# Performance work log

Hardware: AMD Instinct MI355X
Metric: run time of the kernel (lower is better)

## Reference

```python
import jax, jax.numpy as jnp
import numpy as np

HIDDEN = 1280
NUM_HEADS = 20
HEAD_DIM = HIDDEN // NUM_HEADS
B, S = 2, 2048


def setup_inputs() -> dict:
    key = jax.random.key(0)
    k1, k2, k3, k4, k5 = jax.random.split(key, 5)
    scale_in = 1.0 / np.sqrt(HIDDEN)
    return {
        "x": jax.random.normal(k1, (B, S, HIDDEN), dtype=jnp.float32),
        "w_attn": jax.random.normal(k2, (HIDDEN, 3 * HIDDEN), dtype=jnp.float32) * scale_in,
        "b_attn": jax.random.normal(k3, (3 * HIDDEN,), dtype=jnp.float32) * 0.02,
        "w_proj": jax.random.normal(k4, (HIDDEN, HIDDEN), dtype=jnp.float32) * scale_in,
        "b_proj": jax.random.normal(k5, (HIDDEN,), dtype=jnp.float32) * 0.02,
    }


def reference(x, w_attn, b_attn, w_proj, b_proj):
    b, s, _ = x.shape
    scale = 1.0 / np.sqrt(HEAD_DIM)
    qkv = x @ w_attn + b_attn                      # [B,S,3H]
    q, k, v = jnp.split(qkv, 3, axis=-1)

    def heads(t):  # [B,S,H] -> [B,nh,S,hd]
        return t.reshape(b, s, NUM_HEADS, HEAD_DIM).transpose(0, 2, 1, 3)

    q, k, v = heads(q), heads(k), heads(v)
    attn = jnp.einsum("bhqd,bhkd->bhqk", q, k) * scale
    causal = jnp.tril(jnp.ones((s, s), dtype=bool))
    attn = jnp.where(causal, attn, jnp.float32(-jnp.inf))
    attn = jax.nn.softmax(attn, axis=-1)           # dropout = identity (eval)
    out = jnp.einsum("bhqk,bhkd->bhqd", attn, v)
    out = out.transpose(0, 2, 1, 3).reshape(b, s, HIDDEN)
    return out @ w_proj + b_proj
```

## Files before the change

kernel.cpp:

```cpp
#include <hip/hip_runtime.h>

typedef unsigned short u16;
typedef __attribute__((ext_vector_type(8))) short bf16x8;
typedef __attribute__((ext_vector_type(4))) float f32x4;
typedef __attribute__((ext_vector_type(4))) unsigned short u16x4;

#define MFMA16 __builtin_amdgcn_mfma_f32_16x16x32_bf16

__device__ __forceinline__ u16 f2bf(float f) {
  unsigned int u = __float_as_uint(f);
  u += 0x7fff + ((u >> 16) & 1);
  return (u16)(u >> 16);
}

__device__ __forceinline__ float vexp2(float x) {
  float r; asm("v_exp_f32 %0, %1" : "=v"(r) : "v"(x)); return r;
}

template<int CTRL>
__device__ __forceinline__ float dppf(float v) {
  return __int_as_float(__builtin_amdgcn_update_dpp(0, __float_as_int(v), CTRL, 0xF, 0xF, true));
}
__device__ __forceinline__ float rowmax16(float v) {
  v = fmaxf(v, dppf<0xB1>(v));
  v = fmaxf(v, dppf<0x4E>(v));
  v = fmaxf(v, dppf<0x141>(v));
  v = fmaxf(v, dppf<0x140>(v));
  return v;
}
__device__ __forceinline__ float rowsum16(float v) {
  v += dppf<0xB1>(v);
  v += dppf<0x4E>(v);
  v += dppf<0x141>(v);
  v += dppf<0x140>(v);
  return v;
}

__device__ __forceinline__ void gload_lds16(const void* g, void* l) {
  __builtin_amdgcn_global_load_lds((__attribute__((address_space(1))) void*)g,
                                   (__attribute__((address_space(3))) void*)l,
                                   16, 0, 0);
}

__global__ void k_cast(const float* __restrict__ src, u16* __restrict__ dst, int n4) {
  int i = blockIdx.x * 256 + threadIdx.x;
  if (i >= n4) return;
  const float4 v = reinterpret_cast<const float4*>(src)[i];
  u16x4 o = {f2bf(v.x), f2bf(v.y), f2bf(v.z), f2bf(v.w)};
  reinterpret_cast<u16x4*>(dst)[i] = o;
}

__global__ void k_transpose_cast(const float* __restrict__ src, u16* __restrict__ dst,
                                 int R, int C) {
  __shared__ float tile[64][65];
  const int t = threadIdx.x;
  const int c0 = blockIdx.x * 64, r0 = blockIdx.y * 64;
#pragma unroll
  for (int i = 0; i < 16; ++i) {
    int e = i * 256 + t;
    int r = e >> 6, c = e & 63;
    tile[r][c] = src[(size_t)(r0 + r) * C + (c0 + c)];
  }
  __syncthreads();
#pragma unroll
  for (int i = 0; i < 16; ++i) {
    int e = i * 256 + t;
    int r = e >> 6, c = e & 63;
    dst[(size_t)(c0 + r) * R + (r0 + c)] = f2bf(tile[c][r]);
  }
}

__global__ __launch_bounds__(256, 2) void k_gemm_qkv(
    const u16* __restrict__ A, const u16* __restrict__ Bt,
    const float* __restrict__ bias,
    u16* __restrict__ qo, u16* __restrict__ ko, u16* __restrict__ vt) {
  constexpr int K = 1280;
  __shared__ u16 Alds[128 * 64];
  __shared__ u16 Blds[128 * 64];
  const int t = threadIdx.x;
  const int lane = t & 63, wave = t >> 6;
  const int wr = wave >> 1, wc = wave & 1;
  const int l15 = lane & 15, lhi = lane >> 4;
  const int m0 = blockIdx.x * 128, n0 = blockIdx.y * 128;

  f32x4 acc[4][4];
#pragma unroll
  for (int mi = 0; mi < 4; ++mi)
#pragma unroll
    for (int ni = 0; ni < 4; ++ni) acc[mi][ni] = f32x4{0.f, 0.f, 0.f, 0.f};

  const int srow = t >> 3;
  const int scol = (t & 7) * 8;
  const u16* Ag = A + (size_t)(m0 + srow) * K + scol;
  const u16* Bg = Bt + (size_t)(n0 + srow) * K + scol;
  char* Al = (char*)Alds + wave * 1024;
  char* Bl = (char*)Blds + wave * 1024;

  for (int k0 = 0; k0 < K; k0 += 64) {
    __syncthreads();
#pragma unroll
    for (int it = 0; it < 4; ++it) {
      gload_lds16(Ag + (it * 32) * K + k0, Al + it * 4096);
      gload_lds16(Bg + (it * 32) * K + k0, Bl + it * 4096);
    }
    asm volatile("s_waitcnt vmcnt(0)" ::: "memory");
    __syncthreads();
    const u16* Ab = Alds + (wr * 64 + l15) * 64 + lhi * 8;
    const u16* Bb = Blds + (wc * 64 + l15) * 64 + lhi * 8;
    bf16x8 af[4][2], bfv[4][2];
#pragma unroll
    for (int x = 0; x < 4; ++x) {
      af[x][0] = *(const bf16x8*)(Ab + x * 1024);
      af[x][1] = *(const bf16x8*)(Ab + x * 1024 + 32);
      bfv[x][0] = *(const bf16x8*)(Bb + x * 1024);
      bfv[x][1] = *(const bf16x8*)(Bb + x * 1024 + 32);
    }
#pragma unroll
    for (int mi = 0; mi < 4; ++mi)
#pragma unroll
      for (int ni = 0; ni < 4; ++ni) {
        acc[mi][ni] = MFMA16(af[mi][0], bfv[ni][0], acc[mi][ni], 0, 0, 0);
        acc[mi][ni] = MFMA16(af[mi][1], bfv[ni][1], acc[mi][ni], 0, 0, 0);
      }
  }

  const int which = n0 >= 2560 ? 2 : (n0 >= 1280 ? 1 : 0);
  const int bbq = m0 >> 11;
  const int sbase = (m0 & 2047) + wr * 64;
  if (which < 2) {
    u16* outp = which == 0 ? qo : ko;
#pragma unroll
    for (int ni = 0; ni < 4; ++ni) {
      const int n_abs = n0 + wc * 64 + ni * 16 + l15;
      const int nn = n_abs - which * 1280;
      const int h = nn >> 6, d = nn & 63;
      const float bv = bias[n_abs];
#pragma unroll
      for (int mi = 0; mi < 4; ++mi) {
#pragma unroll
        for (int i = 0; i < 4; ++i) {
          const int ss = sbase + mi * 16 + lhi * 4 + i;
          outp[(((size_t)(bbq * 20 + h) * 2048 + ss) << 6) + d] = f2bf(acc[mi][ni][i] + bv);
        }
      }
    }
  } else {
#pragma unroll
    for (int ni = 0; ni < 4; ++ni) {
      const int n_abs = n0 + wc * 64 + ni * 16 + l15;
      const int nn = n_abs - 2560;
      const int h = nn >> 6, d = nn & 63;
      const float bv = bias[n_abs];
      u16* vrow = vt + ((size_t)(bbq * 20 + h) * 64 + d) * 2048;
#pragma unroll
      for (int mi = 0; mi < 4; ++mi) {
        const int ss = sbase + mi * 16 + lhi * 4;
        u16x4 pk = {f2bf(acc[mi][ni][0] + bv), f2bf(acc[mi][ni][1] + bv),
                    f2bf(acc[mi][ni][2] + bv), f2bf(acc[mi][ni][3] + bv)};
        *(u16x4*)(vrow + ss) = pk;
      }
    }
  }
}

__global__ __launch_bounds__(256, 2) void k_gemm_proj(
    const u16* __restrict__ A, const u16* __restrict__ Bt,
    const float* __restrict__ bias, float* __restrict__ out) {
  constexpr int K = 1280;
  __shared__ u16 Alds[128 * 64];
  __shared__ u16 Blds[128 * 64];
  const int t = threadIdx.x;
  const int lane = t & 63, wave = t >> 6;
  const int wr = wave >> 1, wc = wave & 1;
  const int l15 = lane & 15, lhi = lane >> 4;
  const int m0 = blockIdx.x * 128, n0 = blockIdx.y * 128;

  f32x4 acc[4][4];
#pragma unroll
  for (int mi = 0; mi < 4; ++mi)
#pragma unroll
    for (int ni = 0; ni < 4; ++ni) acc[mi][ni] = f32x4{0.f, 0.f, 0.f, 0.f};

  const int srow = t >> 3;
  const int scol = (t & 7) * 8;
  const u16* Ag = A + (size_t)(m0 + srow) * K + scol;
  const u16* Bg = Bt + (size_t)(n0 + srow) * K + scol;
  char* Al = (char*)Alds + wave * 1024;
  char* Bl = (char*)Blds + wave * 1024;

  for (int k0 = 0; k0 < K; k0 += 64) {
    __syncthreads();
#pragma unroll
    for (int it = 0; it < 4; ++it) {
      gload_lds16(Ag + (it * 32) * K + k0, Al + it * 4096);
      gload_lds16(Bg + (it * 32) * K + k0, Bl + it * 4096);
    }
    asm volatile("s_waitcnt vmcnt(0)" ::: "memory");
    __syncthreads();
    const u16* Ab = Alds + (wr * 64 + l15) * 64 + lhi * 8;
    const u16* Bb = Blds + (wc * 64 + l15) * 64 + lhi * 8;
    bf16x8 af[4][2], bfv[4][2];
#pragma unroll
    for (int x = 0; x < 4; ++x) {
      af[x][0] = *(const bf16x8*)(Ab + x * 1024);
      af[x][1] = *(const bf16x8*)(Ab + x * 1024 + 32);
      bfv[x][0] = *(const bf16x8*)(Bb + x * 1024);
      bfv[x][1] = *(const bf16x8*)(Bb + x * 1024 + 32);
    }
#pragma unroll
    for (int mi = 0; mi < 4; ++mi)
#pragma unroll
      for (int ni = 0; ni < 4; ++ni) {
        acc[mi][ni] = MFMA16(af[mi][0], bfv[ni][0], acc[mi][ni], 0, 0, 0);
        acc[mi][ni] = MFMA16(af[mi][1], bfv[ni][1], acc[mi][ni], 0, 0, 0);
      }
  }

#pragma unroll
  for (int ni = 0; ni < 4; ++ni) {
    const int n_abs = n0 + wc * 64 + ni * 16 + l15;
    const float bv = bias[n_abs];
#pragma unroll
    for (int mi = 0; mi < 4; ++mi) {
#pragma unroll
      for (int i = 0; i < 4; ++i) {
        const int m_abs = m0 + wr * 64 + mi * 16 + lhi * 4 + i;
        out[(size_t)m_abs * 1280 + n_abs] = acc[mi][ni][i] + bv;
      }
    }
  }
}

__global__ __launch_bounds__(256, 3) void k_attn8(
    const u16* __restrict__ Qg, const u16* __restrict__ Kg,
    const u16* __restrict__ VT, u16* __restrict__ ao) {
  __shared__ __align__(16) char kvs[2][16384];
  __shared__ u16 Plds[4][32 * 72];
  const int t = threadIdx.x;
  const int lane = t & 63, wave = t >> 6;
  const int l15 = lane & 15, lhi = lane >> 4;
  const int bh = blockIdx.x;
  const int qt = 15 - blockIdx.y;
  const int bb = bh / 20, hh = bh % 20;
  const int q0w = qt * 128 + wave * 32;
  const int nkv = 2 * (qt + 1);
  const size_t base = (size_t)bh * 2048 * 64;
  const size_t vtb = (size_t)bh * 64 * 2048;
  u16* Pw = Plds[wave];

  const int sls = (lane & 7) ^ (lane >> 3);
  const int soff0 = ((lhi ^ (lane & 7)) << 4);
  const int soff1 = (((4 + lhi) ^ (lane & 7)) << 4);

  bf16x8 qf[2][2];
#pragma unroll
  for (int mr = 0; mr < 2; ++mr)
#pragma unroll
    for (int kk = 0; kk < 2; ++kk)
      qf[mr][kk] = *(const bf16x8*)(Qg + base + (size_t)(q0w + mr * 16 + l15) * 64 + kk * 32 + lhi * 8);

  f32x4 o[2][4];
  float m2[2][4], lp[2][4];
#pragma unroll
  for (int mr = 0; mr < 2; ++mr) {
#pragma unroll
    for (int i = 0; i < 4; ++i) { m2[mr][i] = -3.0e38f; lp[mr][i] = 0.f; }
#pragma unroll
    for (int dc = 0; dc < 4; ++dc) o[mr][dc] = f32x4{0.f, 0.f, 0.f, 0.f};
  }
  const float c1 = 0.18033688f;
  const int lastw = (q0w + 31) >> 6;

  auto stage = [&](char* buf, int kv0) {
#pragma unroll
    for (int j = 0; j < 2; ++j) {
      const int r = j * 32 + wave * 8 + (lane >> 3);
      gload_lds16(Kg + base + (size_t)(kv0 + r) * 64 + sls * 8,
                  buf + j * 4096 + wave * 1024);
      gload_lds16(VT + vtb + (size_t)r * 2048 + kv0 + sls * 8,
                  buf + 8192 + j * 4096 + wave * 1024);
    }
  };

  stage(kvs[0], 0);

  for (int tk = 0; tk < nkv; ++tk) {
    const int kv0 = tk * 64;
    if (tk + 1 < nkv) {
      stage(kvs[(tk + 1) & 1], kv0 + 64);
      asm volatile("s_waitcnt vmcnt(4)" ::: "memory");
    } else {
      asm volatile("s_waitcnt vmcnt(0)" ::: "memory");
    }
    __syncthreads();

    if (tk <= lastw) {
      const char* Kb = kvs[tk & 1];
      const char* Vb = kvs[tk & 1] + 8192;
      const char* Krow = Kb + l15 * 128;
      const char* Vrow = Vb + l15 * 128;
      f32x4 sc[2][4];
#pragma unroll
      for (int c = 0; c < 4; ++c) {
        const bf16x8 kf0 = *(const bf16x8*)(Krow + c * 2048 + soff0);
        const bf16x8 kf1 = *(const bf16x8*)(Krow + c * 2048 + soff1);
#pragma unroll
        for (int mr = 0; mr < 2; ++mr) {
          f32x4 z = MFMA16(qf[mr][0], kf0, f32x4{0.f, 0.f, 0.f, 0.f}, 0, 0, 0);
          z = MFMA16(qf[mr][1], kf1, z, 0, 0, 0);
          sc[mr][c] = z;
        }
      }
      if (kv0 + 63 > q0w) {
#pragma unroll
        for (int mr = 0; mr < 2; ++mr)
#pragma unroll
          for (int c = 0; c < 4; ++c)
#pragma unroll
            for (int i = 0; i < 4; ++i) {
              const int qa = q0w + mr * 16 + lhi * 4 + i;
              const int ka = kv0 + c * 16 + l15;
              sc[mr][c][i] = (ka <= qa) ? sc[mr][c][i] : -3.0e38f;
            }
      }
      float tm[2][4];
      bool need = false;
#pragma unroll
      for (int mr = 0; mr < 2; ++mr)
#pragma unroll
        for (int i = 0; i < 4; ++i) {
          float mx = fmaxf(fmaxf(sc[mr][0][i], sc[mr][1][i]),
                           fmaxf(sc[mr][2][i], sc[mr][3][i]));
          mx = rowmax16(mx) * c1;
          tm[mr][i] = mx;
          need |= (mx > m2[mr][i] + 11.5f);
        }
      if (__any(need)) {
#pragma unroll
        for (int mr = 0; mr < 2; ++mr)
#pragma unroll
          for (int i = 0; i < 4; ++i) {
            const float mn = fmaxf(m2[mr][i], tm[mr][i]);
            const float rs = vexp2(m2[mr][i] - mn);
            m2[mr][i] = mn;
            lp[mr][i] *= rs;
#pragma unroll
            for (int dc = 0; dc < 4; ++dc) o[mr][dc][i] *= rs;
          }
      }
#pragma unroll
      for (int mr = 0; mr < 2; ++mr)
#pragma unroll
        for (int i = 0; i < 4; ++i) {
          float psum = 0.f;
#pragma unroll
          for (int c = 0; c < 4; ++c) {
            const float p = vexp2(__builtin_fmaf(sc[mr][c][i], c1, -m2[mr][i]));
            psum += p;
            Pw[(mr * 16 + lhi * 4 + i) * 72 + c * 16 + l15] = f2bf(p);
          }
          lp[mr][i] += psum;
        }
      bf16x8 pf[2][2];
#pragma unroll
      for (int mr = 0; mr < 2; ++mr)
#pragma unroll
        for (int kk = 0; kk < 2; ++kk)
          pf[mr][kk] = *(const bf16x8*)&Pw[(mr * 16 + l15) * 72 + kk * 32 + lhi * 8];
#pragma unroll
      for (int dc = 0; dc < 4; ++dc) {
        const bf16x8 vf0 = *(const bf16x8*)(Vrow + dc * 2048 + soff0);
        const bf16x8 vf1 = *(const bf16x8*)(Vrow + dc * 2048 + soff1);
#pragma unroll
        for (int mr = 0; mr < 2; ++mr) {
          o[mr][dc] = MFMA16(pf[mr][0], vf0, o[mr][dc], 0, 0, 0);
          o[mr][dc] = MFMA16(pf[mr][1], vf1, o[mr][dc], 0, 0, 0);
        }
      }
    }
    __syncthreads();
  }

#pragma unroll
  for (int mr = 0; mr < 2; ++mr)
#pragma unroll
    for (int i = 0; i < 4; ++i) {
      const float lfull = rowsum16(lp[mr][i]);
      const float inv = 1.0f / lfull;
      const int qa = q0w + mr * 16 + lhi * 4 + i;
#pragma unroll
      for (int dc = 0; dc < 4; ++dc) {
        const int d = dc * 16 + l15;
        ao[((size_t)(bb * 2048 + qa)) * 1280 + hh * 64 + d] = f2bf(o[mr][dc][i] * inv);
      }
    }
}

extern "C" void kernel_launch(void* const* d_in, const int* in_sizes, int n_in,
                              void* d_out, int out_size, void* d_ws, size_t ws_size,
                              hipStream_t stream) {
  (void)in_sizes; (void)n_in; (void)out_size; (void)ws_size;
  const float* x      = (const float*)d_in[0];
  const float* w_attn = (const float*)d_in[1];
  const float* b_attn = (const float*)d_in[2];
  const float* w_proj = (const float*)d_in[3];
  const float* b_proj = (const float*)d_in[4];
  float* out = (float*)d_out;

  char* ws = (char*)d_ws;
  u16* x_bf = (u16*)(ws + 0);
  u16* wa_t = (u16*)(ws + 10485760);
  u16* wp_t = (u16*)(ws + 20316160);
  u16* q_ws = (u16*)(ws + 23592960);
  u16* k_ws = (u16*)(ws + 34078720);
  u16* vt   = (u16*)(ws + 44564480);
  u16* ao   = x_bf;

  k_cast<<<5120, 256, 0, stream>>>(x, x_bf, 4096 * 1280 / 4);
  k_transpose_cast<<<dim3(60, 20), 256, 0, stream>>>(w_attn, wa_t, 1280, 3840);
  k_transpose_cast<<<dim3(20, 20), 256, 0, stream>>>(w_proj, wp_t, 1280, 1280);
  k_gemm_qkv<<<dim3(32, 30), 256, 0, stream>>>(x_bf, wa_t, b_attn, q_ws, k_ws, vt);
  k_attn8<<<dim3(40, 16), 256, 0, stream>>>(q_ws, k_ws, vt, ao);
  k_gemm_proj<<<dim3(32, 10), 256, 0, stream>>>(ao, wp_t, b_proj, out);
}
```

Baseline: 166.9 us.

## Make attention kernel persistent with atomic work queue, truncate P to bf16

The attention kernel becomes persistent: 768 blocks repeatedly grab (query-tile, head) units from a global atomic counter, longest causal tiles first. This balances the triangular causal workload across CUs instead of relying on the hardware's static block dispatch. The counter lives in the first word of the output buffer, is zeroed by the QKV GEMM, and is overwritten later by the projection GEMM. Separately, P is converted to bf16 by truncation rather than round-to-nearest, which saves a few ALU ops but adds a small downward bias.

After: 186.7 us. 11.8% more time.

```diff
diff --git a/kernel.cpp b/kernel.cpp
--- a/kernel.cpp
+++ b/kernel.cpp
@@ -73,11 +73,13 @@
 __global__ __launch_bounds__(256, 2) void k_gemm_qkv(
     const u16* __restrict__ A, const u16* __restrict__ Bt,
     const float* __restrict__ bias,
-    u16* __restrict__ qo, u16* __restrict__ ko, u16* __restrict__ vt) {
+    u16* __restrict__ qo, u16* __restrict__ ko, u16* __restrict__ vt,
+    int* __restrict__ ctr) {
   constexpr int K = 1280;
   __shared__ u16 Alds[128 * 64];
   __shared__ u16 Blds[128 * 64];
   const int t = threadIdx.x;
+  if (blockIdx.x == 0 && blockIdx.y == 0 && t == 0) *ctr = 0;
   const int lane = t & 63, wave = t >> 6;
   const int wr = wave >> 1, wc = wave & 1;
   const int l15 = lane & 15, lhi = lane >> 4;
@@ -231,169 +233,176 @@
   }
 }
 
-__global__ __launch_bounds__(256, 3) void k_attn8(
+__global__ __launch_bounds__(256, 3) void k_attn10(
     const u16* __restrict__ Qg, const u16* __restrict__ Kg,
-    const u16* __restrict__ VT, u16* __restrict__ ao) {
+    const u16* __restrict__ VT, u16* __restrict__ ao,
+    int* __restrict__ ctr) {
   __shared__ __align__(16) char kvs[2][16384];
   __shared__ u16 Plds[4][32 * 72];
+  __shared__ int unit_s;
   const int t = threadIdx.x;
   const int lane = t & 63, wave = t >> 6;
   const int l15 = lane & 15, lhi = lane >> 4;
-  const int bh = blockIdx.x;
-  const int qt = 15 - blockIdx.y;
-  const int bb = bh / 20, hh = bh % 20;
-  const int q0w = qt * 128 + wave * 32;
-  const int nkv = 2 * (qt + 1);
-  const size_t base = (size_t)bh * 2048 * 64;
-  const size_t vtb = (size_t)bh * 64 * 2048;
+  const float c1 = 0.18033688f;
   u16* Pw = Plds[wave];
 
   const int sls = (lane & 7) ^ (lane >> 3);
   const int soff0 = ((lhi ^ (lane & 7)) << 4);
   const int soff1 = (((4 + lhi) ^ (lane & 7)) << 4);
 
-  bf16x8 qf[2][2];
-#pragma unroll
-  for (int mr = 0; mr < 2; ++mr)
-#pragma unroll
-    for (int kk = 0; kk < 2; ++kk)
-      qf[mr][kk] = *(const bf16x8*)(Qg + base + (size_t)(q0w + mr * 16 + l15) * 64 + kk * 32 + lhi * 8);
-
-  f32x4 o[2][4];
-  float m2[2][4], lp[2][4];
-#pragma unroll
-  for (int mr = 0; mr < 2; ++mr) {
-#pragma unroll
-    for (int i = 0; i < 4; ++i) { m2[mr][i] = -3.0e38f; lp[mr][i] = 0.f; }
-#pragma unroll
-    for (int dc = 0; dc < 4; ++dc) o[mr][dc] = f32x4{0.f, 0.f, 0.f, 0.f};
-  }
-  const float c1 = 0.18033688f;
-  const int lastw = (q0w + 31) >> 6;
-
-  auto stage = [&](char* buf, int kv0) {
-#pragma unroll
-    for (int j = 0; j < 2; ++j) {
-      const int r = j * 32 + wave * 8 + (lane >> 3);
-      gload_lds16(Kg + base + (size_t)(kv0 + r) * 64 + sls * 8,
-                  buf + j * 4096 + wave * 1024);
-      gload_lds16(VT + vtb + (size_t)r * 2048 + kv0 + sls * 8,
-                  buf + 8192 + j * 4096 + wave * 1024);
-    }
-  };
-
-  stage(kvs[0], 0);
-
-  for (int tk = 0; tk < nkv; ++tk) {
-    const int kv0 = tk * 64;
-    if (tk + 1 < nkv) {
-      stage(kvs[(tk + 1) & 1], kv0 + 64);
-      asm volatile("s_waitcnt vmcnt(4)" ::: "memory");
-    } else {
-      asm volatile("s_waitcnt vmcnt(0)" ::: "memory");
-    }
+  for (;;) {
+    if (t == 0) unit_s = atomicAdd(ctr, 1);
     __syncthreads();
-
-    if (tk <= lastw) {
-      const char* Kb = kvs[tk & 1];
-      const char* Vb = kvs[tk & 1] + 8192;
-      const char* Krow = Kb + l15 * 128;
-      const char* Vrow = Vb + l15 * 128;
-      f32x4 sc[2][4];
-#pragma unroll
-      for (int c = 0; c < 4; ++c) {
-        const bf16x8 kf0 = *(const bf16x8*)(Krow + c * 2048 + soff0);
-        const bf16x8 kf1 = *(const bf16x8*)(Krow + c * 2048 + soff1);
-#pragma unroll
-        for (int mr = 0; mr < 2; ++mr) {
-          f32x4 z = MFMA16(qf[mr][0], kf0, f32x4{0.f, 0.f, 0.f, 0.f}, 0, 0, 0);
-          z = MFMA16(qf[mr][1], kf1, z, 0, 0, 0);
-          sc[mr][c] = z;
-        }
-      }
-      if (kv0 + 63 > q0w) {
+    const int id = unit_s;
+    if (id >= 640) return;
+    const int qt = 15 - id / 40;
+    const int bh = id % 40;
+    const int bb = bh / 20, hh = bh % 20;
+    const int q0w = qt * 128 + wave * 32;
+    const int nkv = 2 * (qt + 1);
+    const size_t base = (size_t)bh * 2048 * 64;
+    const size_t vtb = (size_t)bh * 64 * 2048;
+
+    bf16x8 qf[2][2];
+#pragma unroll
+    for (int mr = 0; mr < 2; ++mr)
+#pragma unroll
+      for (int kk = 0; kk < 2; ++kk)
+        qf[mr][kk] = *(const bf16x8*)(Qg + base + (size_t)(q0w + mr * 16 + l15) * 64 + kk * 32 + lhi * 8);
+
+    f32x4 o[2][4];
+    float m2[2][4], lp[2][4];
+#pragma unroll
+    for (int mr = 0; mr < 2; ++mr) {
+#pragma unroll
+      for (int i = 0; i < 4; ++i) { m2[mr][i] = -3.0e38f; lp[mr][i] = 0.f; }
+#pragma unroll
+      for (int dc = 0; dc < 4; ++dc) o[mr][dc] = f32x4{0.f, 0.f, 0.f, 0.f};
+    }
+    const int lastw = (q0w + 31) >> 6;
+
+    auto stage = [&](char* buf, int kv0) {
+#pragma unroll
+      for (int j = 0; j < 2; ++j) {
+        const int r = j * 32 + wave * 8 + (lane >> 3);
+        gload_lds16(Kg + base + (size_t)(kv0 + r) * 64 + sls * 8,
+                    buf + j * 4096 + wave * 1024);
+        gload_lds16(VT + vtb + (size_t)r * 2048 + kv0 + sls * 8,
+                    buf + 8192 + j * 4096 + wave * 1024);
+      }
+    };
+
+    stage(kvs[0], 0);
+
+    for (int tk = 0; tk < nkv; ++tk) {
+      const int kv0 = tk * 64;
+      if (tk + 1 < nkv) {
+        stage(kvs[(tk + 1) & 1], kv0 + 64);
+        asm volatile("s_waitcnt vmcnt(4)" ::: "memory");
+      } else {
+        asm volatile("s_waitcnt vmcnt(0)" ::: "memory");
+      }
+      __syncthreads();
+
+      if (tk <= lastw) {
+        const char* Krow = kvs[tk & 1] + l15 * 128;
+        const char* Vrow = kvs[tk & 1] + 8192 + l15 * 128;
+        f32x4 sc[2][4];
+#pragma unroll
+        for (int c = 0; c < 4; ++c) {
+          const bf16x8 kf0 = *(const bf16x8*)(Krow + c * 2048 + soff0);
+          const bf16x8 kf1 = *(const bf16x8*)(Krow + c * 2048 + soff1);
+#pragma unroll
+          for (int mr = 0; mr < 2; ++mr) {
+            f32x4 z = MFMA16(qf[mr][0], kf0, f32x4{0.f, 0.f, 0.f, 0.f}, 0, 0, 0);
+            z = MFMA16(qf[mr][1], kf1, z, 0, 0, 0);
+            sc[mr][c] = z;
+          }
+        }
+        if (kv0 + 63 > q0w) {
+#pragma unroll
+          for (int mr = 0; mr < 2; ++mr)
+#pragma unroll
+            for (int c = 0; c < 4; ++c)
+#pragma unroll
+              for (int i = 0; i < 4; ++i) {
+                const int qa = q0w + mr * 16 + lhi * 4 + i;
+                const int ka = kv0 + c * 16 + l15;
+                sc[mr][c][i] = (ka <= qa) ? sc[mr][c][i] : -3.0e38f;
+              }
+        }
+        float tm[2][4];
+        bool need = false;
 #pragma unroll
         for (int mr = 0; mr < 2; ++mr)
 #pragma unroll
-          for (int c = 0; c < 4; ++c)
+          for (int i = 0; i < 4; ++i) {
+            float mx = fmaxf(fmaxf(sc[mr][0][i], sc[mr][1][i]),
+                             fmaxf(sc[mr][2][i], sc[mr][3][i]));
+            mx = rowmax16(mx) * c1;
+            tm[mr][i] = mx;
+            need |= (mx > m2[mr][i] + 11.5f);
+          }
+        if (__any(need)) {
+#pragma unroll
+          for (int mr = 0; mr < 2; ++mr)
 #pragma unroll
             for (int i = 0; i < 4; ++i) {
-              const int qa = q0w + mr * 16 + lhi * 4 + i;
-              const int ka = kv0 + c * 16 + l15;
-              sc[mr][c][i] = (ka <= qa) ? sc[mr][c][i] : -3.0e38f;
+              const float mn = fmaxf(m2[mr][i], tm[mr][i]);
+              const float rs = vexp2(m2[mr][i] - mn);
+              m2[mr][i] = mn;
+              lp[mr][i] *= rs;
+#pragma unroll
+              for (int dc = 0; dc < 4; ++dc) o[mr][dc][i] *= rs;
             }
-      }
-      float tm[2][4];
-      bool need = false;
-#pragma unroll
-      for (int mr = 0; mr < 2; ++mr)
-#pragma unroll
-        for (int i = 0; i < 4; ++i) {
-          float mx = fmaxf(fmaxf(sc[mr][0][i], sc[mr][1][i]),
-                           fmaxf(sc[mr][2][i], sc[mr][3][i]));
-          mx = rowmax16(mx) * c1;
-          tm[mr][i] = mx;
-          need |= (mx > m2[mr][i] + 11.5f);
-        }
-      if (__any(need)) {
+        }
 #pragma unroll
         for (int mr = 0; mr < 2; ++mr)
 #pragma unroll
           for (int i = 0; i < 4; ++i) {
-            const float mn = fmaxf(m2[mr][i], tm[mr][i]);
-            const float rs = vexp2(m2[mr][i] - mn);
-            m2[mr][i] = mn;
-            lp[mr][i] *= rs;
-#pragma unroll
-            for (int dc = 0; dc < 4; ++dc) o[mr][dc][i] *= rs;
+            float psum = 0.f;
+#pragma unroll
+            for (int c = 0; c < 4; ++c) {
+              const float p = vexp2(__builtin_fmaf(sc[mr][c][i], c1, -m2[mr][i]));
+              psum += p;
+              Pw[(mr * 16 + lhi * 4 + i) * 72 + c * 16 + l15] = (u16)(__float_as_uint(p) >> 16);
+            }
+            lp[mr][i] += psum;
           }
-      }
-#pragma unroll
-      for (int mr = 0; mr < 2; ++mr)
-#pragma unroll
-        for (int i = 0; i < 4; ++i) {
-          float psum = 0.f;
-#pragma unroll
-          for (int c = 0; c < 4; ++c) {
-            const float p = vexp2(__builtin_fmaf(sc[mr][c][i], c1, -m2[mr][i]));
-            psum += p;
-            Pw[(mr * 16 + lhi * 4 + i) * 72 + c * 16 + l15] = f2bf(p);
+        bf16x8 pf[2][2];
+#pragma unroll
+        for (int mr = 0; mr < 2; ++mr)
+#pragma unroll
+          for (int kk = 0; kk < 2; ++kk)
+            pf[mr][kk] = *(const bf16x8*)&Pw[(mr * 16 + l15) * 72 + kk * 32 + lhi * 8];
+#pragma unroll
+        for (int dc = 0; dc < 4; ++dc) {
+          const bf16x8 vf0 = *(const bf16x8*)(Vrow + dc * 2048 + soff0);
+          const bf16x8 vf1 = *(const bf16x8*)(Vrow + dc * 2048 + soff1);
+#pragma unroll
+          for (int mr = 0; mr < 2; ++mr) {
+            o[mr][dc] = MFMA16(pf[mr][0], vf0, o[mr][dc], 0, 0, 0);
+            o[mr][dc] = MFMA16(pf[mr][1], vf1, o[mr][dc], 0, 0, 0);
           }
-          lp[mr][i] += psum;
-        }
-      bf16x8 pf[2][2];
-#pragma unroll
-      for (int mr = 0; mr < 2; ++mr)
-#pragma unroll
-        for (int kk = 0; kk < 2; ++kk)
-          pf[mr][kk] = *(const bf16x8*)&Pw[(mr * 16 + l15) * 72 + kk * 32 + lhi * 8];
-#pragma unroll
-      for (int dc = 0; dc < 4; ++dc) {
-        const bf16x8 vf0 = *(const bf16x8*)(Vrow + dc * 2048 + soff0);
-        const bf16x8 vf1 = *(const bf16x8*)(Vrow + dc * 2048 + soff1);
-#pragma unroll
-        for (int mr = 0; mr < 2; ++mr) {
-          o[mr][dc] = MFMA16(pf[mr][0], vf0, o[mr][dc], 0, 0, 0);
-          o[mr][dc] = MFMA16(pf[mr][1], vf1, o[mr][dc], 0, 0, 0);
-        }
-      }
-    }
-    __syncthreads();
-  }
-
-#pragma unroll
-  for (int mr = 0; mr < 2; ++mr)
-#pragma unroll
-    for (int i = 0; i < 4; ++i) {
-      const float lfull = rowsum16(lp[mr][i]);
-      const float inv = 1.0f / lfull;
-      const int qa = q0w + mr * 16 + lhi * 4 + i;
-#pragma unroll
-      for (int dc = 0; dc < 4; ++dc) {
-        const int d = dc * 16 + l15;
-        ao[((size_t)(bb * 2048 + qa)) * 1280 + hh * 64 + d] = f2bf(o[mr][dc][i] * inv);
-      }
-    }
+        }
+      }
+      __syncthreads();
+    }
+
+#pragma unroll
+    for (int mr = 0; mr < 2; ++mr)
+#pragma unroll
+      for (int i = 0; i < 4; ++i) {
+        const float lfull = rowsum16(lp[mr][i]);
+        const float inv = 1.0f / lfull;
+        const int qa = q0w + mr * 16 + lhi * 4 + i;
+#pragma unroll
+        for (int dc = 0; dc < 4; ++dc) {
+          const int d = dc * 16 + l15;
+          ao[((size_t)(bb * 2048 + qa)) * 1280 + hh * 64 + d] = f2bf(o[mr][dc][i] * inv);
+        }
+      }
+  }
 }
 
 extern "C" void kernel_launch(void* const* d_in, const int* in_sizes, int n_in,
@@ -406,6 +415,7 @@
   const float* w_proj = (const float*)d_in[3];
   const float* b_proj = (const float*)d_in[4];
   float* out = (float*)d_out;
+  int* ctr = (int*)d_out;
 
   char* ws = (char*)d_ws;
   u16* x_bf = (u16*)(ws + 0);
@@ -419,7 +429,7 @@
   k_cast<<<5120, 256, 0, stream>>>(x, x_bf, 4096 * 1280 / 4);
   k_transpose_cast<<<dim3(60, 20), 256, 0, stream>>>(w_attn, wa_t, 1280, 3840);
   k_transpose_cast<<<dim3(20, 20), 256, 0, stream>>>(w_proj, wp_t, 1280, 1280);
-  k_gemm_qkv<<<dim3(32, 30), 256, 0, stream>>>(x_bf, wa_t, b_attn, q_ws, k_ws, vt);
-  k_attn8<<<dim3(40, 16), 256, 0, stream>>>(q_ws, k_ws, vt, ao);
+  k_gemm_qkv<<<dim3(32, 30), 256, 0, stream>>>(x_bf, wa_t, b_attn, q_ws, k_ws, vt, ctr);
+  k_attn10<<<768, 256, 0, stream>>>(q_ws, k_ws, vt, ao, ctr);
   k_gemm_proj<<<dim3(32, 10), 256, 0, stream>>>(ao, wp_t, b_proj, out);
 }
```
